# Kernel optimization log

Hardware: AMD Instinct MI355X
Metric: run time of the kernel (lower is better)

The kernel has to match this reference:

```python
import jax, jax.numpy as jnp
import numpy as np

B, C, E = 64, 32, 4
D_MODEL, PRED_LEN = 1024, 720
L_LIST = [32, 16, 8, 4]  # seq_len=512 / patch_sizes [16,32,64,128]
EPS = float(np.finfo(float).eps)


def setup_inputs() -> dict:
    key = jax.random.key(0)
    ks = jax.random.split(key, 16)
    inp = {}
    for i, L in enumerate(L_LIST):
        inp[f"xs{i}"] = jax.random.normal(ks[i], (B, C, L, D_MODEL), dtype=jnp.float32)
    inp["gates"] = jax.random.uniform(ks[4], (B, E), dtype=jnp.float32)
    w_scale = 1.0 / np.sqrt(D_MODEL)
    for i in range(E):
        inp[f"W{i}"] = jax.random.normal(ks[5 + i], (D_MODEL, PRED_LEN), dtype=jnp.float32) * w_scale
        inp[f"b{i}"] = jax.random.normal(ks[9 + i], (PRED_LEN,), dtype=jnp.float32) * 0.01
    return inp


def reference(xs0, xs1, xs2, xs3, gates, W0, b0, W1, b1, W2, b2, W3, b3):
    xs = [xs0, xs1, xs2, xs3]
    Ws = [W0, W1, W2, W3]
    bs = [b0, b1, b2, b3]
    # per-expert linear on last token: [B,C,D] @ [D,P] + [P] -> [B,C,P]
    outs = jnp.stack(
        [jnp.einsum("bcd,dp->bcp", x[:, :, -1, :], W) + b for x, W, b in zip(xs, Ws, bs)]
    )  # [E,B,C,P]
    # dense-gate combine(): sum_e gates[b,e] * exp(out_e[b])
    combined = jnp.einsum("ebcp,be->bcp", jnp.exp(outs), gates)  # [B,C,P]
    combined = jnp.where(combined == 0, EPS, combined)
    out = jnp.log(combined)  # [B,C,P]
    return out.transpose(0, 2, 1)  # 'B C P -> B P C'
```

## Files before the change

### kernel.cpp

```cpp
#include <hip/hip_runtime.h>
#include <hip/hip_bf16.h>


typedef __attribute__((ext_vector_type(4))) float f32x4;
typedef __attribute__((ext_vector_type(8))) short bf16x8;
typedef __attribute__((ext_vector_type(4))) unsigned short u16x4;
typedef __attribute__((ext_vector_type(8))) unsigned short u16x8;

#define EPSV 2.2204460492503131e-16f

__device__ __forceinline__ unsigned short f2bf(float f) {
  unsigned u = __builtin_bit_cast(unsigned, f);
  u += 0x7fffu + ((u >> 16) & 1u);
  return (unsigned short)(u >> 16);
}

__device__ __forceinline__ void gload_lds16(const void* g, void* l) {
  __builtin_amdgcn_global_load_lds(
      (const __attribute__((address_space(1))) unsigned int*)g,
      (__attribute__((address_space(3))) unsigned int*)l, 16, 0, 0);
}

__global__ __launch_bounds__(256) void prep_fused(
    const float* __restrict__ xs0, const float* __restrict__ xs1,
    const float* __restrict__ xs2, const float* __restrict__ xs3,
    const float* __restrict__ W0, const float* __restrict__ W1,
    const float* __restrict__ W2, const float* __restrict__ W3,
    unsigned short* __restrict__ Xb, unsigned short* __restrict__ Wb)
{
  __shared__ __align__(16) unsigned short tile[64 * 72];
  const int tid = threadIdx.x;
  if (blockIdx.x < 4096) {
    const int i = blockIdx.x * 256 + tid;
    const int e = i >> 18;
    const int rem = i & 262143;
    const int m = rem >> 7;
    const int kc = rem & 127;
    const float* xp = (e == 0) ? xs0 : (e == 1) ? xs1 : (e == 2) ? xs2 : xs3;
    const int L = 32 >> e;
    const float* src = xp + ((size_t)m * L + (L - 1)) * 1024 + kc * 8;
    f32x4 v0 = *(const f32x4*)src;
    f32x4 v1 = *(const f32x4*)(src + 4);
    u16x8 pk;
    pk[0] = f2bf(v0[0]); pk[1] = f2bf(v0[1]); pk[2] = f2bf(v0[2]); pk[3] = f2bf(v0[3]);
    pk[4] = f2bf(v1[0]); pk[5] = f2bf(v1[1]); pk[6] = f2bf(v1[2]); pk[7] = f2bf(v1[3]);
    *(u16x8*)(Xb + ((size_t)e * 2048 + m) * 1024 + kc * 8) = pk;
  } else {
    const int wI = blockIdx.x - 4096;
    const int k0 = (wI & 15) * 64;
    const int rest = wI >> 4;
    const int nb = (rest % 12) * 64;
    const int e = rest / 12;
    const float* Wp = (e == 0) ? W0 : (e == 1) ? W1 : (e == 2) ? W2 : W3;
    const int n_c = tid & 15;
    const int r = tid >> 4;
    const int n0 = nb + n_c * 4;
#pragma unroll
    for (int j = 0; j < 4; ++j) {
      const int row = r + j * 16;
      f32x4 v = {0.f, 0.f, 0.f, 0.f};
      if (n0 < 720) v = *(const f32x4*)(Wp + (size_t)(k0 + row) * 720 + n0);
#pragma unroll
      for (int d = 0; d < 4; ++d) tile[(n_c * 4 + d) * 72 + row] = f2bf(v[d]);
    }
    __syncthreads();
    const int n_l = tid >> 2;
    const int kq = tid & 3;
    if (nb + n_l < 720) {
#pragma unroll
      for (int q = 0; q < 2; ++q) {
        const int chunk = q * 4 + kq;
        *(u16x8*)(Wb + ((size_t)e * 720 + nb + n_l) * 1024 + k0 + chunk * 8) =
            *(const u16x8*)(tile + n_l * 72 + chunk * 8);
      }
    }
  }
}

__global__ __launch_bounds__(256) void moe_gemm_e(
    const unsigned short* __restrict__ Xb, const unsigned short* __restrict__ Wb,
    const float* __restrict__ gates,
    const float* __restrict__ b0, const float* __restrict__ b1,
    const float* __restrict__ b2, const float* __restrict__ b3,
    float* __restrict__ planes)
{
  __shared__ __align__(16) unsigned char smem[32768];
  unsigned short* a_lds = (unsigned short*)smem;
  unsigned short* b_lds = (unsigned short*)(smem + 16384);

  const int tid = threadIdx.x;
  const int lane = tid & 63;
  const int wid = tid >> 6;
  const int wm = wid >> 1, wn = wid & 1;

  const int id = ((int)blockIdx.x & 7) * 192 + ((int)blockIdx.x >> 3);
  const int nt = id % 12;
  const int mt = (id / 12) % 32;
  const int e  = id / 384;
  const int nbase = nt * 64;

  const float* barr[4] = {b0, b1, b2, b3};
  const int bI = mt * 2 + wm;
  const float g = gates[bI * 4 + e];
  float bias_r[2];
#pragma unroll
  for (int nf = 0; nf < 2; ++nf) {
    int col = nbase + wn * 32 + nf * 16 + (lane & 15);
    bias_r[nf] = barr[e][col < 720 ? col : 719];
  }

  const unsigned short* asrc = Xb + (size_t)e * 2048 * 1024 + (size_t)mt * 64 * 1024;
  const unsigned short* bsrc = Wb + (size_t)e * 720 * 1024;

  auto stage = [&](int k0, int buf) {
#pragma unroll
    for (int j = 0; j < 2; ++j) {
      const int C = j * 256 + tid;
      const int row = C >> 3, c = C & 7;
      gload_lds16(asrc + (size_t)row * 1024 + k0 + ((c ^ (row & 7)) * 8),
                  a_lds + buf * 4096 + C * 8);
    }
#pragma unroll
    for (int j = 0; j < 2; ++j) {
      const int C = j * 256 + tid;
      const int row = C >> 3, c = C & 7;
      int n = nbase + row; if (n > 719) n = 719;
      gload_lds16(bsrc + (size_t)n * 1024 + k0 + ((c ^ (row & 7)) * 8),
                  b_lds + buf * 4096 + C * 8);
    }
  };

  auto compute = [&](int buf, f32x4 (&acc)[2][2]) {
    const unsigned short* al = a_lds + buf * 4096;
    const unsigned short* bl = b_lds + buf * 4096;
#pragma unroll
    for (int ks = 0; ks < 2; ++ks) {
      const int kb = ks * 64 + (lane >> 4) * 16;
      bf16x8 af[2], bfm[2];
#pragma unroll
      for (int mf = 0; mf < 2; ++mf) {
        const int r = wm * 32 + mf * 16 + (lane & 15);
        const int byte = (r * 128 + kb) ^ ((r & 7) << 4);
        af[mf] = *(const bf16x8*)((const char*)al + byte);
      }
#pragma unroll
      for (int nf = 0; nf < 2; ++nf) {
        const int r = wn * 32 + nf * 16 + (lane & 15);
        const int byte = (r * 128 + kb) ^ ((r & 7) << 4);
        bfm[nf] = *(const bf16x8*)((const char*)bl + byte);
      }
#pragma unroll
      for (int mf = 0; mf < 2; ++mf)
#pragma unroll
        for (int nf = 0; nf < 2; ++nf)
          acc[mf][nf] = __builtin_amdgcn_mfma_f32_16x16x32_bf16(
              af[mf], bfm[nf], acc[mf][nf], 0, 0, 0);
    }
  };

  f32x4 acc[2][2] = {};
  int cur = 0;
  stage(0, 0);
  __syncthreads();
  for (int kt = 0; kt < 16; ++kt) {
    if (kt < 15) stage((kt + 1) * 64, cur ^ 1);
    compute(cur, acc);
    __syncthreads();
    cur ^= 1;
  }

#pragma unroll
  for (int nf = 0; nf < 2; ++nf) {
    const int p = nbase + wn * 32 + nf * 16 + (lane & 15);
    if (p < 720) {
#pragma unroll
      for (int mf = 0; mf < 2; ++mf) {
        const int m0 = mt * 64 + wm * 32 + mf * 16 + ((lane >> 4) << 2);
        float* dst = planes + ((size_t)e * 2048 + m0) * 720 + p;
#pragma unroll
        for (int j = 0; j < 4; ++j)
          dst[j * 720] = g * __expf(acc[mf][nf][j] + bias_r[nf]);
      }
    }
  }
}

__global__ __launch_bounds__(128) void reduce_log(
    const float* __restrict__ planes, float* __restrict__ out)
{
  __shared__ __align__(16) float t[64 * 36];
  const int nt = blockIdx.x;
  const int b  = blockIdx.y;
  const int nbase = nt * 64;
  const int tid = threadIdx.x;

#pragma unroll
  for (int it = 0; it < 4; ++it) {
    const int i = it * 128 + tid;
    const int row = i >> 4;
    const int pc = i & 15;
    int p0 = nbase + pc * 4;
    if (p0 > 716) p0 = 716;
    const size_t base = ((size_t)b * 32 + row) * 720 + p0;
    f32x4 s = *(const f32x4*)(planes + base);
    s += *(const f32x4*)(planes + (size_t)2048 * 720 + base);
    s += *(const f32x4*)(planes + (size_t)2 * 2048 * 720 + base);
    s += *(const f32x4*)(planes + (size_t)3 * 2048 * 720 + base);
#pragma unroll
    for (int d = 0; d < 4; ++d) {
      float v = s[d];
      v = (v == 0.0f) ? EPSV : v;
      t[(pc * 4 + d) * 36 + row] = __logf(v);
    }
  }
  __syncthreads();
#pragma unroll
  for (int it = 0; it < 4; ++it) {
    const int i = it * 128 + tid;
    const int p_l = i >> 3;
    const int cc = i & 7;
    const int p = nbase + p_l;
    if (p < 720) {
      f32x4 v = *(const f32x4*)(t + p_l * 36 + cc * 4);
      *(f32x4*)(out + ((size_t)b * 720 + p) * 32 + cc * 4) = v;
    }
  }
}

__global__ __launch_bounds__(256) void moe_head_fallback(
    const float* __restrict__ xs0, const float* __restrict__ xs1,
    const float* __restrict__ xs2, const float* __restrict__ xs3,
    const float* __restrict__ gates,
    const float* __restrict__ W0, const float* __restrict__ b0,
    const float* __restrict__ W1, const float* __restrict__ b1,
    const float* __restrict__ W2, const float* __restrict__ b2,
    const float* __restrict__ W3, const float* __restrict__ b3,
    float* __restrict__ out)
{
  __shared__ __align__(16) unsigned short a_lds[64 * 64];
  __shared__ __align__(16) unsigned short b_lds[64 * 64];
  __shared__ __align__(16) float t_lds[4][32 * 36];
  const int tid = threadIdx.x;
  const int lane = tid & 63;
  const int wid = tid >> 6;
  const int wm = wid >> 1, wn = wid & 1;
  const int nt = blockIdx.x, mt = blockIdx.y;
  const int mbase = mt * 64, nbase = nt * 64;
  const float* xarr[4] = {xs0, xs1, xs2, xs3};
  const float* Warr[4] = {W0, W1, W2, W3};
  const float* barr[4] = {b0, b1, b2, b3};
  constexpr int Larr[4] = {32, 16, 8, 4};
  f32x4 comb[2][2] = {};
#pragma unroll
  for (int e = 0; e < 4; ++e) {
    const int L = Larr[e];
    const float* xlast = xarr[e] + (size_t)(L - 1) * 1024;
    const size_t xstride = (size_t)L * 1024;
    const float* Wp = Warr[e];
    f32x4 acc[2][2] = {};
    for (int kt = 0; kt < 16; ++kt) {
      const int k0 = kt * 64;
      __syncthreads();
      {
        const int k_l = (tid & 15) * 4;
        const int r0 = tid >> 4;
#pragma unroll
        for (int j = 0; j < 4; ++j) {
          const int row = r0 + j * 16;
          f32x4 v = *(const f32x4*)(xlast + (size_t)(mbase + row) * xstride + (k0 + k_l));
          u16x4 pk;
          pk[0] = f2bf(v[0]); pk[1] = f2bf(v[1]); pk[2] = f2bf(v[2]); pk[3] = f2bf(v[3]);
          const int byte = (row * 128 + k_l * 2) ^ ((row & 7) << 4);
          *(u16x4*)((char*)a_lds + byte) = pk;
        }
      }
      {
        const int n_l = tid & 63;
        const int kq = tid >> 6;
        const int n_g = nbase + n_l;
        const bool nok = (n_g < 720);
        const float* wcol = Wp + n_g;
#pragma unroll
        for (int g = 0; g < 4; ++g) {
          const int k_l = kq * 4 + g * 16;
          float w0 = 0.f, w1 = 0.f, w2 = 0.f, w3 = 0.f;
          if (nok) {
            const float* s = wcol + (size_t)(k0 + k_l) * 720;
            w0 = s[0]; w1 = s[720]; w2 = s[1440]; w3 = s[2160];
          }
          u16x4 pk;
          pk[0] = f2bf(w0); pk[1] = f2bf(w1); pk[2] = f2bf(w2); pk[3] = f2bf(w3);
          const int byte = (n_l * 128 + k_l * 2) ^ ((n_l & 7) << 4);
          *(u16x4*)((char*)b_lds + byte) = pk;
        }
      }
      __syncthreads();
#pragma unroll
      for (int ks = 0; ks < 2; ++ks) {
        const int kb2 = (ks * 32 + (lane >> 4) * 8) * 2;
        bf16x8 af[2], bfr[2];
#pragma unroll
        for (int mf = 0; mf < 2; ++mf) {
          const int r = wm * 32 + mf * 16 + (lane & 15);
          const int byte = (r * 128 + kb2) ^ ((r & 7) << 4);
          af[mf] = *(const bf16x8*)((const char*)a_lds + byte);
        }
#pragma unroll
        for (int nf = 0; nf < 2; ++nf) {
          const int r = wn * 32 + nf * 16 + (lane & 15);
          const int byte = (r * 128 + kb2) ^ ((r & 7) << 4);
          bfr[nf] = *(const bf16x8*)((const char*)b_lds + byte);
        }
#pragma unroll
        for (int mf = 0; mf < 2; ++mf)
#pragma unroll
          for (int nf = 0; nf < 2; ++nf)
            acc[mf][nf] = __builtin_amdgcn_mfma_f32_16x16x32_bf16(
                af[mf], bfr[nf], acc[mf][nf], 0, 0, 0);
      }
    }
    {
      const int b_idx = mt * 2 + wm;
      const float g = gates[b_idx * 4 + e];
#pragma unroll
      for (int nf = 0; nf < 2; ++nf) {
        const int col = nbase + wn * 32 + nf * 16 + (lane & 15);
        const float bias = (col < 720) ? barr[e][col] : 0.0f;
#pragma unroll
        for (int mf = 0; mf < 2; ++mf)
#pragma unroll
          for (int j = 0; j < 4; ++j)
            comb[mf][nf][j] += g * __expf(acc[mf][nf][j] + bias);
      }
    }
  }
  {
    float* tl = &t_lds[wid][0];
#pragma unroll
    for (int mf = 0; mf < 2; ++mf)
#pragma unroll
      for (int nf = 0; nf < 2; ++nf)
#pragma unroll
        for (int j = 0; j < 4; ++j) {
          const int row_l = mf * 16 + (lane >> 4) * 4 + j;
          const int col_l = nf * 16 + (lane & 15);
          float v = comb[mf][nf][j];
          v = (v == 0.0f) ? EPSV : v;
          tl[col_l * 36 + row_l] = __logf(v);
        }
    __syncthreads();
    const int b_idx = mt * 2 + wm;
    const int pbase = nbase + wn * 32;
#pragma unroll
    for (int it = 0; it < 4; ++it) {
      const int p_l = it * 8 + (lane >> 3);
      const int p = pbase + p_l;
      if (p < 720) {
        f32x4 v = *(const f32x4*)(tl + p_l * 36 + (lane & 7) * 4);
        *(f32x4*)(out + ((size_t)b_idx * 720 + p) * 32 + (lane & 7) * 4) = v;
      }
    }
  }
}

extern "C" void kernel_launch(void* const* d_in, const int* in_sizes, int n_in,
                              void* d_out, int out_size, void* d_ws, size_t ws_size,
                              hipStream_t stream) {
  const size_t xb_elems = (size_t)4 * 2048 * 1024;
  const size_t wb_elems = (size_t)4 * 720 * 1024;
  const size_t plane_elems = (size_t)4 * 2048 * 720;
  const size_t need = (xb_elems + wb_elems) * 2 + plane_elems * 4;
  if (ws_size >= need) {
    unsigned short* Xb = (unsigned short*)d_ws;
    unsigned short* Wb = Xb + xb_elems;
    float* planes = (float*)(Wb + wb_elems);
    prep_fused<<<4096 + 768, 256, 0, stream>>>(
        (const float*)d_in[0], (const float*)d_in[1],
        (const float*)d_in[2], (const float*)d_in[3],
        (const float*)d_in[5], (const float*)d_in[7],
        (const float*)d_in[9], (const float*)d_in[11],
        Xb, Wb);
    moe_gemm_e<<<1536, 256, 0, stream>>>(
        Xb, Wb, (const float*)d_in[4],
        (const float*)d_in[6], (const float*)d_in[8],
        (const float*)d_in[10], (const float*)d_in[12],
        planes);
    reduce_log<<<dim3(12, 64), 128, 0, stream>>>(planes, (float*)d_out);
  } else {
    moe_head_fallback<<<dim3(12, 32), 256, 0, stream>>>(
        (const float*)d_in[0], (const float*)d_in[1],
        (const float*)d_in[2], (const float*)d_in[3],
        (const float*)d_in[4],
        (const float*)d_in[5], (const float*)d_in[6],
        (const float*)d_in[7], (const float*)d_in[8],
        (const float*)d_in[9], (const float*)d_in[10],
        (const float*)d_in[11], (const float*)d_in[12],
        (float*)d_out);
  }
}
```

Baseline: 45.27 us.

## Store gated exp planes in bf16 and double GEMM M-tile to 128

```diff
diff --git a/kernel.cpp b/kernel.cpp
--- a/kernel.cpp
+++ b/kernel.cpp
@@ -13,6 +13,10 @@
   unsigned u = __builtin_bit_cast(unsigned, f);
   u += 0x7fffu + ((u >> 16) & 1u);
   return (unsigned short)(u >> 16);
+}
+__device__ __forceinline__ float bf2f(unsigned short h) {
+  unsigned u = ((unsigned)h) << 16;
+  return __builtin_bit_cast(float, u);
 }
 
 __device__ __forceinline__ void gload_lds16(const void* g, void* l) {
@@ -82,26 +86,28 @@
     const float* __restrict__ gates,
     const float* __restrict__ b0, const float* __restrict__ b1,
     const float* __restrict__ b2, const float* __restrict__ b3,
-    float* __restrict__ planes)
+    unsigned short* __restrict__ planes)
 {
-  __shared__ __align__(16) unsigned char smem[32768];
+  __shared__ __align__(16) unsigned char smem[49152];
   unsigned short* a_lds = (unsigned short*)smem;
-  unsigned short* b_lds = (unsigned short*)(smem + 16384);
+  unsigned short* b_lds = (unsigned short*)(smem + 32768);
 
   const int tid = threadIdx.x;
   const int lane = tid & 63;
   const int wid = tid >> 6;
   const int wm = wid >> 1, wn = wid & 1;
 
-  const int id = ((int)blockIdx.x & 7) * 192 + ((int)blockIdx.x >> 3);
+  const int id = ((int)blockIdx.x & 7) * 96 + ((int)blockIdx.x >> 3);
   const int nt = id % 12;
-  const int mt = (id / 12) % 32;
-  const int e  = id / 384;
+  const int mt = (id / 12) % 16;
+  const int e  = id / 192;
   const int nbase = nt * 64;
 
   const float* barr[4] = {b0, b1, b2, b3};
-  const int bI = mt * 2 + wm;
-  const float g = gates[bI * 4 + e];
+  float g_r[2];
+#pragma unroll
+  for (int h = 0; h < 2; ++h)
+    g_r[h] = gates[(mt * 4 + wm * 2 + h) * 4 + e];
   float bias_r[2];
 #pragma unroll
   for (int nf = 0; nf < 2; ++nf) {
@@ -109,16 +115,16 @@
     bias_r[nf] = barr[e][col < 720 ? col : 719];
   }
 
-  const unsigned short* asrc = Xb + (size_t)e * 2048 * 1024 + (size_t)mt * 64 * 1024;
+  const unsigned short* asrc = Xb + (size_t)e * 2048 * 1024 + (size_t)mt * 128 * 1024;
   const unsigned short* bsrc = Wb + (size_t)e * 720 * 1024;
 
   auto stage = [&](int k0, int buf) {
 #pragma unroll
-    for (int j = 0; j < 2; ++j) {
+    for (int j = 0; j < 4; ++j) {
       const int C = j * 256 + tid;
       const int row = C >> 3, c = C & 7;
       gload_lds16(asrc + (size_t)row * 1024 + k0 + ((c ^ (row & 7)) * 8),
-                  a_lds + buf * 4096 + C * 8);
+                  a_lds + buf * 8192 + C * 8);
     }
 #pragma unroll
     for (int j = 0; j < 2; ++j) {
@@ -130,16 +136,16 @@
     }
   };
 
-  auto compute = [&](int buf, f32x4 (&acc)[2][2]) {
-    const unsigned short* al = a_lds + buf * 4096;
+  auto compute = [&](int buf, f32x4 (&acc)[4][2]) {
+    const unsigned short* al = a_lds + buf * 8192;
     const unsigned short* bl = b_lds + buf * 4096;
 #pragma unroll
     for (int ks = 0; ks < 2; ++ks) {
       const int kb = ks * 64 + (lane >> 4) * 16;
-      bf16x8 af[2], bfm[2];
-#pragma unroll
-      for (int mf = 0; mf < 2; ++mf) {
-        const int r = wm * 32 + mf * 16 + (lane & 15);
+      bf16x8 af[4], bfm[2];
+#pragma unroll
+      for (int mf = 0; mf < 4; ++mf) {
+        const int r = wm * 64 + mf * 16 + (lane & 15);
         const int byte = (r * 128 + kb) ^ ((r & 7) << 4);
         af[mf] = *(const bf16x8*)((const char*)al + byte);
       }
@@ -150,7 +156,7 @@
         bfm[nf] = *(const bf16x8*)((const char*)bl + byte);
       }
 #pragma unroll
-      for (int mf = 0; mf < 2; ++mf)
+      for (int mf = 0; mf < 4; ++mf)
 #pragma unroll
         for (int nf = 0; nf < 2; ++nf)
           acc[mf][nf] = __builtin_amdgcn_mfma_f32_16x16x32_bf16(
@@ -158,7 +164,7 @@
     }
   };
 
-  f32x4 acc[2][2] = {};
+  f32x4 acc[4][2] = {};
   int cur = 0;
   stage(0, 0);
   __syncthreads();
@@ -174,19 +180,20 @@
     const int p = nbase + wn * 32 + nf * 16 + (lane & 15);
     if (p < 720) {
 #pragma unroll
-      for (int mf = 0; mf < 2; ++mf) {
-        const int m0 = mt * 64 + wm * 32 + mf * 16 + ((lane >> 4) << 2);
-        float* dst = planes + ((size_t)e * 2048 + m0) * 720 + p;
+      for (int mf = 0; mf < 4; ++mf) {
+        const int m0 = mt * 128 + wm * 64 + mf * 16 + ((lane >> 4) << 2);
+        const float g = g_r[mf >> 1];
+        unsigned short* dst = planes + ((size_t)e * 2048 + m0) * 720 + p;
 #pragma unroll
         for (int j = 0; j < 4; ++j)
-          dst[j * 720] = g * __expf(acc[mf][nf][j] + bias_r[nf]);
-      }
-    }
-  }
-}
-
-__global__ __launch_bounds__(128) void reduce_log(
-    const float* __restrict__ planes, float* __restrict__ out)
+          dst[j * 720] = f2bf(g * __expf(acc[mf][nf][j] + bias_r[nf]));
+      }
+    }
+  }
+}
+
+__global__ __launch_bounds__(256) void reduce_log(
+    const unsigned short* __restrict__ planes, float* __restrict__ out)
 {
   __shared__ __align__(16) float t[64 * 36];
   const int nt = blockIdx.x;
@@ -194,29 +201,31 @@
   const int nbase = nt * 64;
   const int tid = threadIdx.x;
 
-#pragma unroll
-  for (int it = 0; it < 4; ++it) {
-    const int i = it * 128 + tid;
-    const int row = i >> 4;
-    const int pc = i & 15;
-    int p0 = nbase + pc * 4;
-    if (p0 > 716) p0 = 716;
+  {
+    const int row = tid >> 3;
+    const int pc = tid & 7;
+    int p0 = nbase + pc * 8;
+    if (p0 > 712) p0 = 712;
     const size_t base = ((size_t)b * 32 + row) * 720 + p0;
-    f32x4 s = *(const f32x4*)(planes + base);
-    s += *(const f32x4*)(planes + (size_t)2048 * 720 + base);
-    s += *(const f32x4*)(planes + (size_t)2 * 2048 * 720 + base);
-    s += *(const f32x4*)(planes + (size_t)3 * 2048 * 720 + base);
-#pragma unroll
-    for (int d = 0; d < 4; ++d) {
+    float s[8] = {};
+#pragma unroll
+    for (int pl = 0; pl < 4; ++pl) {
+      u16x8 v = *(const u16x8*)(planes + (size_t)pl * 2048 * 720 + base);
+#pragma unroll
+      for (int d = 0; d < 8; ++d) s[d] += bf2f(v[d]);
+    }
+    const int pbase_l = (p0 - nbase);
+#pragma unroll
+    for (int d = 0; d < 8; ++d) {
       float v = s[d];
       v = (v == 0.0f) ? EPSV : v;
-      t[(pc * 4 + d) * 36 + row] = __logf(v);
+      t[(pbase_l + d) * 36 + row] = __logf(v);
     }
   }
   __syncthreads();
 #pragma unroll
-  for (int it = 0; it < 4; ++it) {
-    const int i = it * 128 + tid;
+  for (int it = 0; it < 2; ++it) {
+    const int i = it * 256 + tid;
     const int p_l = i >> 3;
     const int cc = i & 7;
     const int p = nbase + p_l;
@@ -369,23 +378,23 @@
   const size_t xb_elems = (size_t)4 * 2048 * 1024;
   const size_t wb_elems = (size_t)4 * 720 * 1024;
   const size_t plane_elems = (size_t)4 * 2048 * 720;
-  const size_t need = (xb_elems + wb_elems) * 2 + plane_elems * 4;
+  const size_t need = (xb_elems + wb_elems + plane_elems) * 2;
   if (ws_size >= need) {
     unsigned short* Xb = (unsigned short*)d_ws;
     unsigned short* Wb = Xb + xb_elems;
-    float* planes = (float*)(Wb + wb_elems);
+    unsigned short* planes = Wb + wb_elems;
     prep_fused<<<4096 + 768, 256, 0, stream>>>(
         (const float*)d_in[0], (const float*)d_in[1],
         (const float*)d_in[2], (const float*)d_in[3],
         (const float*)d_in[5], (const float*)d_in[7],
         (const float*)d_in[9], (const float*)d_in[11],
         Xb, Wb);
-    moe_gemm_e<<<1536, 256, 0, stream>>>(
+    moe_gemm_e<<<768, 256, 0, stream>>>(
         Xb, Wb, (const float*)d_in[4],
         (const float*)d_in[6], (const float*)d_in[8],
         (const float*)d_in[10], (const float*)d_in[12],
         planes);
-    reduce_log<<<dim3(12, 64), 128, 0, stream>>>(planes, (float*)d_out);
+    reduce_log<<<dim3(12, 64), 256, 0, stream>>>(planes, (float*)d_out);
   } else {
     moe_head_fallback<<<dim3(12, 32), 256, 0, stream>>>(
         (const float*)d_in[0], (const float*)d_in[1],
```

Measured after the change: 39.71 us. -12.3%, faster.
